# Optimization experiments

Hardware: AMD Instinct MI355X
Metric: run time of the kernel (lower is better)

The kernel has to match this reference:

```python
import jax, jax.numpy as jnp
import numpy as np

B, C, D = 32, 24, 12          # batch, feature channels, spatial grid
Q_DIM = 11                    # hardcoded question dim in original (k*2+11)
K = C + 2                     # channels after coordinate concat
G_IN = 2 * K + Q_DIM          # 63
G_HID = 256
F_OUT = 10


def setup_inputs() -> dict:
    key = jax.random.key(0)
    ks = jax.random.split(key, 7)
    s = lambda fan_in: 1.0 / np.sqrt(fan_in)
    return {
        "image": jax.random.normal(ks[0], (B, C, D, D), jnp.float32),
        "question": jax.random.normal(ks[1], (B, Q_DIM), jnp.float32),
        "Wg1": jax.random.normal(ks[2], (G_IN, G_HID), jnp.float32) * s(G_IN),
        "bg1": jnp.zeros((G_HID,), jnp.float32),
        "Wg2": jax.random.normal(ks[3], (G_HID, G_HID), jnp.float32) * s(G_HID),
        "bg2": jnp.zeros((G_HID,), jnp.float32),
        "Wf1": jax.random.normal(ks[4], (G_HID, G_HID), jnp.float32) * s(G_HID),
        "bf1": jnp.zeros((G_HID,), jnp.float32),
        "Wf2": jax.random.normal(ks[5], (G_HID, F_OUT), jnp.float32) * s(G_HID),
        "bf2": jnp.zeros((F_OUT,), jnp.float32),
    }


def reference(image, question, Wg1, bg1, Wg2, bg2, Wf1, bf1, Wf2, bf2):
    b, c, d, _ = image.shape
    # coordinate channels: torch.arange(0, 1+1e-5, 1/(d-1)) == linspace(0,1,d)
    coord = jnp.linspace(0.0, 1.0, d, dtype=image.dtype)
    cx = jnp.broadcast_to(coord[None, None, None, :], (b, 1, d, d))
    cy = jnp.broadcast_to(coord[None, None, :, None], (b, 1, d, d))
    x = jnp.concatenate([image, cx, cy], axis=1)            # [b, k, d, d]
    k = c + 2
    n = d * d
    x = x.reshape(b, k, n).transpose(0, 2, 1)                # [b, n, k] objects
    # all-pairs construction: left repeats objects along axis 1, right along axis 2
    x_left = jnp.broadcast_to(x[:, None, :, :], (b, n, n, k)).reshape(b, n * n, k)
    x_right = jnp.broadcast_to(x[:, :, None, :], (b, n, n, k)).reshape(b, n * n, k)
    q = jnp.broadcast_to(question[:, None, :], (b, n * n, question.shape[1]))
    pairs = jnp.concatenate([x_left, x_right, q], axis=2)    # [b, n^2, 2k+11]
    # shared MLP g per pair
    h = jax.nn.relu(jnp.einsum('bpi,ih->bph', pairs, Wg1) + bg1)
    h = jax.nn.relu(jnp.einsum('bph,ho->bpo', h, Wg2) + bg2)
    s = h.sum(axis=1)                                        # [b, 256] sum over pairs
    # MLP f
    o = jax.nn.relu(s @ Wf1 + bf1)
    return o @ Wf2 + bf2                                     # [b, 10]
```

## Files before the change

### kernel.cpp

```cpp
#include <hip/hip_runtime.h>
#include <hip/hip_bf16.h>

#define NB   32
#define NC   24
#define ND   12
#define NN   144
#define QD   11
#define GH   256
#define FOUT 10

typedef unsigned short u16;
typedef _Float16 f16;
typedef __attribute__((ext_vector_type(8))) _Float16 f16x8;
typedef __attribute__((ext_vector_type(4))) float f32x4;

#define LQ_U16  0
#define R_U16   1179648
#define BS_U16  2359296
#define S_BYTE  4849664

__device__ inline u16 f2h(float f) {
  f16 h = (f16)f;
  return *reinterpret_cast<u16*>(&h);
}

__global__ __launch_bounds__(256) void prep(const float* __restrict__ image,
                                            const float* __restrict__ question,
                                            const float* __restrict__ Wg1,
                                            const float* __restrict__ bg1,
                                            const float* __restrict__ Wg2,
                                            u16* __restrict__ Lq,
                                            u16* __restrict__ R,
                                            float* __restrict__ S,
                                            u16* __restrict__ Bswz) {
  int blk = blockIdx.x;
  int h   = threadIdx.x;
  if (blk < 256) {
    const int quarter = blk & 3;
    const int b       = (blk >> 2) & 31;
    const int which   = blk >> 7;
    float Wl[NC + 2];
#pragma unroll
    for (int r = 0; r < NC + 2; ++r)
      Wl[r] = Wg1[(which * (NC + 2) + r) * GH + h];
    float qacc = 0.f;
    if (which == 0) {
      qacc = bg1[h];
#pragma unroll
      for (int tq = 0; tq < QD; ++tq)
        qacc += question[b * QD + tq] * Wg1[(2 * (NC + 2) + tq) * GH + h];
    }
    const float* img = image + b * (NC * NN);
    u16* dst = (which == 0 ? Lq : R) + b * NN * GH + h;
    const float inv = 1.0f / (ND - 1);
#pragma unroll 4
    for (int p = quarter * 36; p < quarter * 36 + 36; ++p) {
      float acc = qacc;
#pragma unroll
      for (int c = 0; c < NC; ++c) acc += img[c * NN + p] * Wl[c];
      int i = p / ND, j = p - i * ND;
      acc += (j * inv) * Wl[24];
      acc += (i * inv) * Wl[25];
      dst[p * GH] = f2h(acc);
    }
  } else {
    int tid = (blk - 256) * 256 + h;
    int e   = tid & 7;
    int l   = (tid >> 3) & 63;
    int fid = tid >> 9;
    int kt  = fid >> 4, nt = fid & 15;
    int k = kt * 32 + ((l >> 4) << 3) + e;
    int n = (nt << 4) + (l & 15);
    Bswz[tid] = f2h(Wg2[k * GH + n]);
    if (tid < NB * GH) S[tid] = 0.f;
  }
}

__global__ __launch_bounds__(512, 2) void pair_gemm(const u16* __restrict__ Lq,
                                                    const u16* __restrict__ R,
                                                    const u16* __restrict__ Bswz,
                                                    const float* __restrict__ bg2,
                                                    float* __restrict__ S) {
  const int bid = blockIdx.x;
  const int xcd = bid & 7;
  const int idx = bid >> 3;
  const int b   = xcd * 4 + (idx >> 4);
  const int bi  = idx & 15;
  const int t0  = bi * 10 + (bi < 2 ? bi : 2);
  const int cnt = 10 + (bi < 2 ? 1 : 0);

  __shared__ __align__(16) u16 As[8 * 8 * 64 * 8];

  const int t = threadIdx.x;
  const int w = t >> 6, l = t & 63;
  const int wn = w & 3, wm = w >> 2;
  const int brow = t >> 2;
  const int oc   = t & 3;
  const int mf_w   = brow >> 4;
  const int lane_w = ((brow & 15) | (oc << 4)) ^ (oc << 1);
  const int lane_r = l ^ (((l >> 4) & 3) << 1);

  const u16* Lbase = Lq + b * NN * GH;
  const u16* Rbase = R + b * NN * GH;
  const u16* Bl    = Bswz + l * 8;

  float bgv[4];
#pragma unroll
  for (int nt = 0; nt < 4; ++nt)
    bgv[nt] = bg2[(wn << 6) + (nt << 4) + (l & 15)];
  float ssum[4] = {0.f, 0.f, 0.f, 0.f};

  for (int tt = 0; tt < cnt; ++tt) {
    {
      int p = (t0 + tt) * 128 + brow;
      int i = p / NN, j = p - i * NN;
      const u16* Lr = Lbase + i * GH + oc * 8;
      const u16* Rr = Rbase + j * GH + oc * 8;
#pragma unroll
      for (int half = 0; half < 2; ++half) {
        f16x8 lv[4], rv[4];
#pragma unroll
        for (int q = 0; q < 4; ++q) {
          lv[q] = *(const f16x8*)(Lr + ((half << 2) | q) * 32);
          rv[q] = *(const f16x8*)(Rr + ((half << 2) | q) * 32);
        }
#pragma unroll
        for (int q = 0; q < 4; ++q) {
          const int kt = (half << 2) | q;
          f16x8 s = lv[q] + rv[q];
          s = __builtin_elementwise_max(s, (f16x8)0.0f);
          *(f16x8*)&As[((((kt << 3) | mf_w) << 6) | lane_w) << 3] = s;
        }
      }
    }
    __syncthreads();

    f32x4 acc[4][4] = {};
#pragma unroll
    for (int kt = 0; kt < 8; ++kt) {
      f16x8 af[4];
#pragma unroll
      for (int mf = 0; mf < 4; ++mf)
        af[mf] = *(const f16x8*)
            &As[((((kt << 3) | (wm << 2) | mf) << 6) | lane_r) << 3];
      f16x8 bfr[4];
#pragma unroll
      for (int nt = 0; nt < 4; ++nt) {
        int fid = (kt << 4) | (wn << 2) | nt;
        bfr[nt] = *(const f16x8*)(Bl + ((size_t)fid << 9));
      }
      __builtin_amdgcn_s_setprio(1);
#pragma unroll
      for (int mf = 0; mf < 4; ++mf)
#pragma unroll
        for (int nt = 0; nt < 4; ++nt)
          acc[mf][nt] = __builtin_amdgcn_mfma_f32_16x16x32_f16(
              af[mf], bfr[nt], acc[mf][nt], 0, 0, 0);
      __builtin_amdgcn_s_setprio(0);
    }
#pragma unroll
    for (int nt = 0; nt < 4; ++nt) {
      float s = 0.f;
#pragma unroll
      for (int mf = 0; mf < 4; ++mf)
#pragma unroll
        for (int r = 0; r < 4; ++r) {
          float v = acc[mf][nt][r] + bgv[nt];
          s += v > 0.f ? v : 0.f;
        }
      ssum[nt] += s;
    }
    __syncthreads();
  }

  float* Sb = S + b * GH;
#pragma unroll
  for (int nt = 0; nt < 4; ++nt) {
    float s = ssum[nt];
    s += __shfl_xor(s, 16, 64);
    s += __shfl_xor(s, 32, 64);
    if (l < 16) atomicAdd(&Sb[(wn << 6) + (nt << 4) + l], s);
  }
}

__global__ __launch_bounds__(256) void final_mlp(const float* __restrict__ S,
                                                 const float* __restrict__ Wf1,
                                                 const float* __restrict__ bf1,
                                                 const float* __restrict__ Wf2,
                                                 const float* __restrict__ bf2,
                                                 float* __restrict__ out) {
  __shared__ float sS[GH];
  __shared__ float oS[GH];
  int b = blockIdx.x, h = threadIdx.x;
  sS[h] = S[b * GH + h];
  __syncthreads();
  float acc = bf1[h];
#pragma unroll 8
  for (int k = 0; k < GH; ++k) acc += sS[k] * Wf1[k * GH + h];
  oS[h] = acc > 0.f ? acc : 0.f;
  __syncthreads();
  if (h < FOUT) {
    float o = bf2[h];
#pragma unroll 8
    for (int k = 0; k < GH; ++k) o += oS[k] * Wf2[k * FOUT + h];
    out[b * FOUT + h] = o;
  }
}

extern "C" void kernel_launch(void* const* d_in, const int* in_sizes, int n_in,
                              void* d_out, int out_size, void* d_ws, size_t ws_size,
                              hipStream_t stream) {
  const float* image    = (const float*)d_in[0];
  const float* question = (const float*)d_in[1];
  const float* Wg1      = (const float*)d_in[2];
  const float* bg1      = (const float*)d_in[3];
  const float* Wg2      = (const float*)d_in[4];
  const float* bg2      = (const float*)d_in[5];
  const float* Wf1      = (const float*)d_in[6];
  const float* bf1      = (const float*)d_in[7];
  const float* Wf2      = (const float*)d_in[8];
  const float* bf2      = (const float*)d_in[9];
  float* out = (float*)d_out;

  u16*   wsb  = (u16*)d_ws;
  u16*   Lqp  = wsb + LQ_U16;
  u16*   Rp   = wsb + R_U16;
  u16*   Bswz = wsb + BS_U16;
  float* Sp   = (float*)((char*)d_ws + S_BYTE);

  prep<<<512, 256, 0, stream>>>(image, question, Wg1, bg1, Wg2,
                                Lqp, Rp, Sp, Bswz);
  pair_gemm<<<512, 512, 0, stream>>>(Lqp, Rp, Bswz, bg2, Sp);
  final_mlp<<<NB, 256, 0, stream>>>(Sp, Wf1, bf1, Wf2, bf2, out);
}
```

Measured before the change: 105.5 us.

## Prefetch next tile's R rows and next k-step B fragments in registers

The R-row loads for the next pair tile are issued right after the barrier, so they overlap the MFMA loop instead of sitting on the critical path of the A-tile build. The j index is tracked incrementally, since it advances by 128 mod 144 each tile. Wg2 fragments are also double-buffered, loading the next k-step's B fragments before issuing the current MFMAs. This raises register pressure, with 32 extra VGPRs for Rpre and 16 for bnxt, which may hurt occupancy under launch_bounds(512,2).

Result: slower. 129.7 us (+22.9%).

```diff
diff --git a/kernel.cpp b/kernel.cpp
--- a/kernel.cpp
+++ b/kernel.cpp
@@ -110,53 +110,65 @@
     bgv[nt] = bg2[(wn << 6) + (nt << 4) + (l & 15)];
   float ssum[4] = {0.f, 0.f, 0.f, 0.f};
 
+  int pj = (t0 * 128 + brow) % NN;
+  f16x8 Rpre[8];
+  {
+    const u16* Rr = Rbase + pj * GH + oc * 8;
+#pragma unroll
+    for (int u = 0; u < 8; ++u)
+      Rpre[u] = *(const f16x8*)(Rr + u * 32);
+  }
+  f16x8 bcur[4], bnxt[4];
+#pragma unroll
+  for (int nt = 0; nt < 4; ++nt)
+    bcur[nt] = *(const f16x8*)(Bl + ((size_t)((wn << 2) | nt) << 9));
+
   for (int tt = 0; tt < cnt; ++tt) {
     {
       int p = (t0 + tt) * 128 + brow;
-      int i = p / NN, j = p - i * NN;
+      int i = p / NN;
       const u16* Lr = Lbase + i * GH + oc * 8;
-      const u16* Rr = Rbase + j * GH + oc * 8;
-#pragma unroll
-      for (int half = 0; half < 2; ++half) {
-        f16x8 lv[4], rv[4];
-#pragma unroll
-        for (int q = 0; q < 4; ++q) {
-          lv[q] = *(const f16x8*)(Lr + ((half << 2) | q) * 32);
-          rv[q] = *(const f16x8*)(Rr + ((half << 2) | q) * 32);
-        }
-#pragma unroll
-        for (int q = 0; q < 4; ++q) {
-          const int kt = (half << 2) | q;
-          f16x8 s = lv[q] + rv[q];
-          s = __builtin_elementwise_max(s, (f16x8)0.0f);
-          *(f16x8*)&As[((((kt << 3) | mf_w) << 6) | lane_w) << 3] = s;
-        }
+#pragma unroll
+      for (int u = 0; u < 8; ++u) {
+        f16x8 lv = *(const f16x8*)(Lr + u * 32);
+        f16x8 s  = lv + Rpre[u];
+        s = __builtin_elementwise_max(s, (f16x8)0.0f);
+        *(f16x8*)&As[((((u << 3) | mf_w) << 6) | lane_w) << 3] = s;
       }
     }
     __syncthreads();
 
+    if (tt + 1 < cnt) {
+      pj = (pj >= 16) ? pj - 16 : pj + 128;
+      const u16* Rr = Rbase + pj * GH + oc * 8;
+#pragma unroll
+      for (int u = 0; u < 8; ++u)
+        Rpre[u] = *(const f16x8*)(Rr + u * 32);
+    }
+
     f32x4 acc[4][4] = {};
 #pragma unroll
     for (int kt = 0; kt < 8; ++kt) {
+#pragma unroll
+      for (int nt = 0; nt < 4; ++nt) {
+        int fid = (((kt + 1) & 7) << 4) | (wn << 2) | nt;
+        bnxt[nt] = *(const f16x8*)(Bl + ((size_t)fid << 9));
+      }
       f16x8 af[4];
 #pragma unroll
       for (int mf = 0; mf < 4; ++mf)
         af[mf] = *(const f16x8*)
             &As[((((kt << 3) | (wm << 2) | mf) << 6) | lane_r) << 3];
-      f16x8 bfr[4];
-#pragma unroll
-      for (int nt = 0; nt < 4; ++nt) {
-        int fid = (kt << 4) | (wn << 2) | nt;
-        bfr[nt] = *(const f16x8*)(Bl + ((size_t)fid << 9));
-      }
       __builtin_amdgcn_s_setprio(1);
 #pragma unroll
       for (int mf = 0; mf < 4; ++mf)
 #pragma unroll
         for (int nt = 0; nt < 4; ++nt)
           acc[mf][nt] = __builtin_amdgcn_mfma_f32_16x16x32_f16(
-              af[mf], bfr[nt], acc[mf][nt], 0, 0, 0);
+              af[mf], bcur[nt], acc[mf][nt], 0, 0, 0);
       __builtin_amdgcn_s_setprio(0);
+#pragma unroll
+      for (int nt = 0; nt < 4; ++nt) bcur[nt] = bnxt[nt];
     }
 #pragma unroll
     for (int nt = 0; nt < 4; ++nt) {
```
